# Optimization experiments

Measured on AMD Instinct MI355X. Metric: run time of the kernel, lower is better.

The kernel has to match this reference:

```python
import jax, jax.numpy as jnp
import numpy as np

B, T, J, D = 64, 2048, 128, 512


def setup_inputs() -> dict:
    key = jax.random.key(0)
    k1, k2, k3, k4 = jax.random.split(key, 4)
    question = jax.random.normal(k1, (B, J, D), dtype=jnp.float32)
    context = jax.random.normal(k2, (B, T, D), dtype=jnp.float32)
    question_len = jax.random.randint(k3, (B,), 1, J + 1, dtype=jnp.int32)
    context_len = jax.random.randint(k4, (B,), 1, T + 1, dtype=jnp.int32)
    weight = jnp.ones((D, 1), dtype=jnp.float32)  # initializer='ones'
    return {"question": question, "context": context,
            "question_len": question_len, "context_len": context_len,
            "weight": weight}


def reference(question, context, question_len, context_len, weight):
    # Original computes sum_d context[b,t,d]*question[b,j,d]*w[d] via a
    # broadcast [B,T,J,D] intermediate; reformulated as a batched GEMM.
    w = weight[:, 0]                                   # [D]
    sim = jnp.einsum('btd,bjd->btj', context * w, question)  # [B,T,J]
    Jm = question.shape[1]
    Tm = context.shape[1]
    q_mask = (jnp.arange(Jm) < question_len[:, None]).astype(jnp.float32)  # [B,J]
    c_mask = (jnp.arange(Tm) < context_len[:, None]).astype(jnp.float32)   # [B,T]
    mask = c_mask[:, :, None] * q_mask[:, None, :]     # [B,T,J]
    neg = jnp.finfo(jnp.float32).min
    sim = sim + neg * (1.0 - mask)
    attn = jax.nn.softmax(sim, axis=1)                 # softmax over context axis T
    return jnp.sum(attn * mask, axis=2)[..., None]     # [B,T,1]
```

## Files before the change

### kernel.cpp

```cpp
#include <hip/hip_runtime.h>
#include <stdint.h>
#include <math.h>

#define BB 64
#define TT 2048
#define JJ 128
#define DD 512
#define BK 32

typedef short short8 __attribute__((ext_vector_type(8)));
typedef float f32x4 __attribute__((ext_vector_type(4)));

typedef const __attribute__((address_space(1))) uint32_t glb_u32;
typedef __attribute__((address_space(3))) uint32_t lds_u32;

__device__ __forceinline__ void dma16(const void* g, void* l) {
  __builtin_amdgcn_global_load_lds((glb_u32*)g, (lds_u32*)l, 16, 0, 0);
}

__device__ inline unsigned pk_hi(float a, float b) {
  return __builtin_amdgcn_perm(__float_as_uint(b), __float_as_uint(a), 0x07060302u);
}
__device__ inline float truncbf(float x) {
  return __uint_as_float(__float_as_uint(x) & 0xFFFF0000u);
}
__device__ inline void pack8(float4 a, float4 b, uint4& h, uint4& l) {
  h = make_uint4(pk_hi(a.x, a.y), pk_hi(a.z, a.w), pk_hi(b.x, b.y), pk_hi(b.z, b.w));
  float l0 = a.x - truncbf(a.x), l1 = a.y - truncbf(a.y);
  float l2 = a.z - truncbf(a.z), l3 = a.w - truncbf(a.w);
  float l4 = b.x - truncbf(b.x), l5 = b.y - truncbf(b.y);
  float l6 = b.z - truncbf(b.z), l7 = b.w - truncbf(b.w);
  l = make_uint4(pk_hi(l0, l1), pk_hi(l2, l3), pk_hi(l4, l5), pk_hi(l6, l7));
}
__device__ inline short8 bc8(uint4 u) { return __builtin_bit_cast(short8, u); }

__global__ __launch_bounds__(256)
void qpack_kernel(const float* __restrict__ Qm, const float* __restrict__ w,
                  uint4* __restrict__ Qhi, uint4* __restrict__ Qlo) {
  const int gid = blockIdx.x * 256 + threadIdx.x;
  const int c = gid & 3;
  const int ks = (gid >> 2) & 15;
  const int j = (gid >> 6) & 127;
  const int b = gid >> 13;
  const float* qp = Qm + (((size_t)b * JJ + j) * DD) + ks * BK + c * 8;
  const float* wp = w + ks * BK + c * 8;
  float4 a = *(const float4*)qp;
  float4 bq = *(const float4*)(qp + 4);
  float4 wa = *(const float4*)wp;
  float4 wb = *(const float4*)(wp + 4);
  a.x *= wa.x; a.y *= wa.y; a.z *= wa.z; a.w *= wa.w;
  bq.x *= wb.x; bq.y *= wb.y; bq.z *= wb.z; bq.w *= wb.w;
  uint4 h, l;
  pack8(a, bq, h, l);
  const int slot = j * 4 + (c ^ ((j >> 1) & 3));
  const size_t o = ((size_t)(b * 16 + ks)) * 512 + slot;
  Qhi[o] = h;
  Qlo[o] = l;
}

__global__ __launch_bounds__(256, 3)
void sim_gemm_mfma(const uint4* __restrict__ Qhi, const uint4* __restrict__ Qlo,
                   const float* __restrict__ Cm, const int* __restrict__ qlen,
                   const int* __restrict__ clen, float* __restrict__ S) {
  __shared__ uint4 Ah[512];
  __shared__ uint4 Al[512];
  __shared__ uint4 Cl[1024];

  const int id = blockIdx.x;
  const int nid = (id & 7) * 128 + (id >> 3);
  const int b = nid >> 4;
  const int t0 = (nid & 15) * 128;

  const int cl = clen[b];
  if (t0 >= cl) return;
  const int ql = qlen[b];

  const int tid = threadIdx.x;
  const int lane = tid & 63;
  const int wv = tid >> 6;

  const uint4* qh_src = Qhi + (size_t)b * 8192 + wv * 128 + lane;
  const uint4* ql_src = Qlo + (size_t)b * 8192 + wv * 128 + lane;
  char* ah_dst = (char*)Ah + wv * 2048;
  char* al_dst = (char*)Al + wv * 2048;
  const int crow = wv * 32 + (lane >> 3);
  const int cch = (lane & 7) ^ ((lane >> 3) & 7);
  const float* c_src = Cm + ((size_t)b * TT + t0 + crow) * DD + cch * 4;
  char* cl_dst = (char*)Cl + wv * 4096;

  const int wm = (wv & 1) * 64;
  const int wn = (wv >> 1) * 64;
  const int l15 = lane & 15;
  const int q = lane >> 4;
  const int fchunk = q ^ ((l15 >> 1) & 3);
  const int swl = l15 & 7;

  bool mact[4];
#pragma unroll
  for (int i = 0; i < 4; i++) mact[i] = (wm + i * 16) < ql;
  const bool any_m = mact[0];

  int aslot[4];
#pragma unroll
  for (int i = 0; i < 4; i++) aslot[i] = (wm + i * 16 + l15) * 4 + fchunk;

  f32x4 acc[4][4] = {};

  for (int ks = 0; ks < 16; ks++) {
    __syncthreads();
#pragma unroll
    for (int s = 0; s < 2; s++) {
      dma16(qh_src + ks * 512 + s * 64, ah_dst + s * 1024);
      dma16(ql_src + ks * 512 + s * 64, al_dst + s * 1024);
    }
#pragma unroll
    for (int s = 0; s < 4; s++) {
      dma16(c_src + (size_t)ks * BK + s * 8 * DD, cl_dst + s * 1024);
    }
    __syncthreads();

    if (!any_m) continue;

    short8 bh[4], bl[4];
#pragma unroll
    for (int ni = 0; ni < 4; ni++) {
      const int row = wn + ni * 16 + l15;
      float4 v0 = __builtin_bit_cast(float4, Cl[row * 8 + ((2 * q) ^ swl)]);
      float4 v1 = __builtin_bit_cast(float4, Cl[row * 8 + ((2 * q + 1) ^ swl)]);
      uint4 h, l;
      pack8(v0, v1, h, l);
      bh[ni] = bc8(h);
      bl[ni] = bc8(l);
    }
#pragma unroll
    for (int mi = 0; mi < 4; mi++) {
      if (!mact[mi]) continue;
      short8 ah = bc8(Ah[aslot[mi]]);
      short8 al = bc8(Al[aslot[mi]]);
#pragma unroll
      for (int ni = 0; ni < 4; ni++) {
        acc[mi][ni] = __builtin_amdgcn_mfma_f32_16x16x32_bf16(ah, bh[ni], acc[mi][ni], 0, 0, 0);
        acc[mi][ni] = __builtin_amdgcn_mfma_f32_16x16x32_bf16(al, bh[ni], acc[mi][ni], 0, 0, 0);
        acc[mi][ni] = __builtin_amdgcn_mfma_f32_16x16x32_bf16(ah, bl[ni], acc[mi][ni], 0, 0, 0);
      }
    }
  }

#pragma unroll
  for (int mi = 0; mi < 4; mi++) {
    if (!mact[mi]) continue;
#pragma unroll
    for (int ni = 0; ni < 4; ni++) {
      const int j = wm + mi * 16 + q * 4;
      const int t = t0 + wn + ni * 16 + l15;
      float* dst = S + ((size_t)b * JJ + j) * TT + t;
      dst[0 * TT] = acc[mi][ni][0];
      dst[1 * TT] = acc[mi][ni][1];
      dst[2 * TT] = acc[mi][ni][2];
      dst[3 * TT] = acc[mi][ni][3];
    }
  }
}

__global__ __launch_bounds__(256)
void softmax_stats_kernel(const float* __restrict__ S, const int* __restrict__ qlen,
                          const int* __restrict__ clen, float* __restrict__ m_out,
                          float* __restrict__ r_out) {
  const int j = blockIdx.x;
  const int b = blockIdx.y;
  if (j >= qlen[b]) return;
  const int cl = clen[b];
  const int tid = threadIdx.x;
  const float4* row = (const float4*)(S + ((size_t)b * JJ + j) * TT);

  const float NEG = -3.4e38f;
  float4 v0 = make_float4(NEG, NEG, NEG, NEG);
  float4 v1 = make_float4(NEG, NEG, NEG, NEG);
  const int t0 = tid * 4;
  const int t1 = (tid + 256) * 4;
  if (t0 < cl) v0 = row[tid];
  if (t1 < cl) v1 = row[tid + 256];

  float m = NEG;
  m = fmaxf(m, (t0 + 0 < cl) ? v0.x : NEG);
  m = fmaxf(m, (t0 + 1 < cl) ? v0.y : NEG);
  m = fmaxf(m, (t0 + 2 < cl) ? v0.z : NEG);
  m = fmaxf(m, (t0 + 3 < cl) ? v0.w : NEG);
  m = fmaxf(m, (t1 + 0 < cl) ? v1.x : NEG);
  m = fmaxf(m, (t1 + 1 < cl) ? v1.y : NEG);
  m = fmaxf(m, (t1 + 2 < cl) ? v1.z : NEG);
  m = fmaxf(m, (t1 + 3 < cl) ? v1.w : NEG);

  __shared__ float red[8];
#pragma unroll
  for (int off = 32; off > 0; off >>= 1) m = fmaxf(m, __shfl_down(m, off));
  if ((tid & 63) == 0) red[tid >> 6] = m;
  __syncthreads();
  m = fmaxf(fmaxf(red[0], red[1]), fmaxf(red[2], red[3]));

  float s = 0.f;
  s += (t0 + 0 < cl) ? __expf(v0.x - m) : 0.f;
  s += (t0 + 1 < cl) ? __expf(v0.y - m) : 0.f;
  s += (t0 + 2 < cl) ? __expf(v0.z - m) : 0.f;
  s += (t0 + 3 < cl) ? __expf(v0.w - m) : 0.f;
  s += (t1 + 0 < cl) ? __expf(v1.x - m) : 0.f;
  s += (t1 + 1 < cl) ? __expf(v1.y - m) : 0.f;
  s += (t1 + 2 < cl) ? __expf(v1.z - m) : 0.f;
  s += (t1 + 3 < cl) ? __expf(v1.w - m) : 0.f;
#pragma unroll
  for (int off = 32; off > 0; off >>= 1) s += __shfl_down(s, off);
  if ((tid & 63) == 0) red[4 + (tid >> 6)] = s;
  __syncthreads();
  s = red[4] + red[5] + red[6] + red[7];

  if (tid == 0) {
    m_out[(size_t)b * JJ + j] = m;
    r_out[(size_t)b * JJ + j] = 1.f / s;
  }
}

__global__ __launch_bounds__(256)
void out_kernel(const float* __restrict__ S, const float* __restrict__ m_arr,
                const float* __restrict__ r_arr, const int* __restrict__ qlen,
                const int* __restrict__ clen, float* __restrict__ out) {
  const int b = blockIdx.y;
  const int t = blockIdx.x * 256 + threadIdx.x;
  const int ql = qlen[b];
  const int cl = clen[b];

  __shared__ float lm[JJ];
  __shared__ float lr[JJ];
  if (threadIdx.x < ql) {
    lm[threadIdx.x] = m_arr[(size_t)b * JJ + threadIdx.x];
    lr[threadIdx.x] = r_arr[(size_t)b * JJ + threadIdx.x];
  }
  __syncthreads();

  float acc = 0.f;
  if (t < cl) {
    const float* col = S + (size_t)b * JJ * TT + t;
#pragma unroll 4
    for (int j = 0; j < ql; j++) {
      acc += __expf(col[(size_t)j * TT] - lm[j]) * lr[j];
    }
  }
  out[(size_t)b * TT + t] = acc;
}

extern "C" void kernel_launch(void* const* d_in, const int* in_sizes, int n_in,
                              void* d_out, int out_size, void* d_ws, size_t ws_size,
                              hipStream_t stream) {
  const float* question = (const float*)d_in[0];
  const float* context  = (const float*)d_in[1];
  const int*   qlen     = (const int*)d_in[2];
  const int*   clen     = (const int*)d_in[3];
  const float* weight   = (const float*)d_in[4];
  float* out = (float*)d_out;

  float* S = (float*)d_ws;
  float* m_arr = S + (size_t)BB * JJ * TT;
  float* r_arr = m_arr + (size_t)BB * JJ;
  uint4* Qhi = (uint4*)(r_arr + (size_t)BB * JJ);
  uint4* Qlo = Qhi + (size_t)BB * 16 * 512;

  qpack_kernel<<<dim3(2048), 256, 0, stream>>>(question, weight, Qhi, Qlo);
  sim_gemm_mfma<<<dim3(1024), 256, 0, stream>>>(Qhi, Qlo, context, qlen, clen, S);
  softmax_stats_kernel<<<dim3(JJ, BB), 256, 0, stream>>>(S, qlen, clen, m_arr, r_arr);
  out_kernel<<<dim3(TT / 256, BB), 256, 0, stream>>>(S, m_arr, r_arr, qlen, clen, out);
}
```

Measured before the change: 393.6 us.

## Load GEMM operands directly from global into registers, dropping LDS staging

The similarity GEMM no longer stages Q and context tiles through shared memory with async global-to-LDS copies and barriers. Each wave now loads its own MFMA fragments straight from global memory into registers. The Q pre-pack kernel writes fragments in the exact per-lane order the MFMA expects, so those reads are contiguous. This removes the block-wide synchronisation and lets waves with no valid question rows exit early. In exchange, context data that two waves share is read twice from global or cache, context loads are less coalesced, and launch bounds drop to 1, which may raise register use and change occupancy.

```diff
diff --git a/kernel.cpp b/kernel.cpp
--- a/kernel.cpp
+++ b/kernel.cpp
@@ -10,13 +10,6 @@
 
 typedef short short8 __attribute__((ext_vector_type(8)));
 typedef float f32x4 __attribute__((ext_vector_type(4)));
-
-typedef const __attribute__((address_space(1))) uint32_t glb_u32;
-typedef __attribute__((address_space(3))) uint32_t lds_u32;
-
-__device__ __forceinline__ void dma16(const void* g, void* l) {
-  __builtin_amdgcn_global_load_lds((glb_u32*)g, (lds_u32*)l, 16, 0, 0);
-}
 
 __device__ inline unsigned pk_hi(float a, float b) {
   return __builtin_amdgcn_perm(__float_as_uint(b), __float_as_uint(a), 0x07060302u);
@@ -38,11 +31,15 @@
 void qpack_kernel(const float* __restrict__ Qm, const float* __restrict__ w,
                   uint4* __restrict__ Qhi, uint4* __restrict__ Qlo) {
   const int gid = blockIdx.x * 256 + threadIdx.x;
-  const int c = gid & 3;
-  const int ks = (gid >> 2) & 15;
-  const int j = (gid >> 6) & 127;
+  const int lane = gid & 63;
+  const int mi = (gid >> 6) & 3;
+  const int str = (gid >> 8) & 1;
+  const int ks = (gid >> 9) & 15;
   const int b = gid >> 13;
-  const float* qp = Qm + (((size_t)b * JJ + j) * DD) + ks * BK + c * 8;
+  const int j = str * 64 + mi * 16 + (lane & 15);
+  const int c = lane >> 4;
+
+  const float* qp = Qm + ((size_t)b * JJ + j) * DD + ks * BK + c * 8;
   const float* wp = w + ks * BK + c * 8;
   float4 a = *(const float4*)qp;
   float4 bq = *(const float4*)(qp + 4);
@@ -52,20 +49,14 @@
   bq.x *= wb.x; bq.y *= wb.y; bq.z *= wb.z; bq.w *= wb.w;
   uint4 h, l;
   pack8(a, bq, h, l);
-  const int slot = j * 4 + (c ^ ((j >> 1) & 3));
-  const size_t o = ((size_t)(b * 16 + ks)) * 512 + slot;
-  Qhi[o] = h;
-  Qlo[o] = l;
-}
-
-__global__ __launch_bounds__(256, 3)
+  Qhi[gid] = h;
+  Qlo[gid] = l;
+}
+
+__global__ __launch_bounds__(256, 1)
 void sim_gemm_mfma(const uint4* __restrict__ Qhi, const uint4* __restrict__ Qlo,
                    const float* __restrict__ Cm, const int* __restrict__ qlen,
                    const int* __restrict__ clen, float* __restrict__ S) {
-  __shared__ uint4 Ah[512];
-  __shared__ uint4 Al[512];
-  __shared__ uint4 Cl[1024];
-
   const int id = blockIdx.x;
   const int nid = (id & 7) * 128 + (id >> 3);
   const int b = nid >> 4;
@@ -78,65 +69,51 @@
   const int tid = threadIdx.x;
   const int lane = tid & 63;
   const int wv = tid >> 6;
-
-  const uint4* qh_src = Qhi + (size_t)b * 8192 + wv * 128 + lane;
-  const uint4* ql_src = Qlo + (size_t)b * 8192 + wv * 128 + lane;
-  char* ah_dst = (char*)Ah + wv * 2048;
-  char* al_dst = (char*)Al + wv * 2048;
-  const int crow = wv * 32 + (lane >> 3);
-  const int cch = (lane & 7) ^ ((lane >> 3) & 7);
-  const float* c_src = Cm + ((size_t)b * TT + t0 + crow) * DD + cch * 4;
-  char* cl_dst = (char*)Cl + wv * 4096;
-
   const int wm = (wv & 1) * 64;
   const int wn = (wv >> 1) * 64;
   const int l15 = lane & 15;
   const int q = lane >> 4;
-  const int fchunk = q ^ ((l15 >> 1) & 3);
-  const int swl = l15 & 7;
 
   bool mact[4];
 #pragma unroll
   for (int i = 0; i < 4; i++) mact[i] = (wm + i * 16) < ql;
-  const bool any_m = mact[0];
-
-  int aslot[4];
-#pragma unroll
-  for (int i = 0; i < 4; i++) aslot[i] = (wm + i * 16 + l15) * 4 + fchunk;
+  if (!mact[0]) return;
+
+  const uint4* ahp = Qhi + (size_t)b * 8192 + (wv & 1) * 256 + lane;
+  const uint4* alp = Qlo + (size_t)b * 8192 + (wv & 1) * 256 + lane;
+  const float* cb = Cm + ((size_t)b * TT + t0 + wn + l15) * DD + q * 8;
 
   f32x4 acc[4][4] = {};
 
   for (int ks = 0; ks < 16; ks++) {
-    __syncthreads();
-#pragma unroll
-    for (int s = 0; s < 2; s++) {
-      dma16(qh_src + ks * 512 + s * 64, ah_dst + s * 1024);
-      dma16(ql_src + ks * 512 + s * 64, al_dst + s * 1024);
-    }
-#pragma unroll
-    for (int s = 0; s < 4; s++) {
-      dma16(c_src + (size_t)ks * BK + s * 8 * DD, cl_dst + s * 1024);
-    }
-    __syncthreads();
-
-    if (!any_m) continue;
-
+    float4 cv0[4], cv1[4];
+#pragma unroll
+    for (int ni = 0; ni < 4; ni++) {
+      const float* cp = cb + ni * 16 * DD + ks * BK;
+      cv0[ni] = *(const float4*)cp;
+      cv1[ni] = *(const float4*)(cp + 4);
+    }
+    uint4 ahv[4], alv[4];
+#pragma unroll
+    for (int mi = 0; mi < 4; mi++) {
+      if (mact[mi]) {
+        ahv[mi] = ahp[ks * 512 + mi * 64];
+        alv[mi] = alp[ks * 512 + mi * 64];
+      }
+    }
     short8 bh[4], bl[4];
 #pragma unroll
     for (int ni = 0; ni < 4; ni++) {
-      const int row = wn + ni * 16 + l15;
-      float4 v0 = __builtin_bit_cast(float4, Cl[row * 8 + ((2 * q) ^ swl)]);
-      float4 v1 = __builtin_bit_cast(float4, Cl[row * 8 + ((2 * q + 1) ^ swl)]);
       uint4 h, l;
-      pack8(v0, v1, h, l);
+      pack8(cv0[ni], cv1[ni], h, l);
       bh[ni] = bc8(h);
       bl[ni] = bc8(l);
     }
 #pragma unroll
     for (int mi = 0; mi < 4; mi++) {
       if (!mact[mi]) continue;
-      short8 ah = bc8(Ah[aslot[mi]]);
-      short8 al = bc8(Al[aslot[mi]]);
+      short8 ah = bc8(ahv[mi]);
+      short8 al = bc8(alv[mi]);
 #pragma unroll
       for (int ni = 0; ni < 4; ni++) {
         acc[mi][ni] = __builtin_amdgcn_mfma_f32_16x16x32_bf16(ah, bh[ni], acc[mi][ni], 0, 0, 0);
```

New measurement: 397.6 us. About the same (+1.0%).

## Fuse per-tile softmax max/sum into GEMM epilogue and merge partials online

Applied to the files above, without the earlier changes.

The GEMM epilogue now computes per-tile row max and exp-sum from the accumulators using shuffles and shared memory, writing (max,sum) partials per 128-column tile. A small merge kernel combines the partials with an online-softmax rescale, replacing the stats kernel that re-read the full similarity matrix. This removes one full pass over S from global memory, at the cost of extra epilogue work, barriers, and register pressure in the GEMM kernel.

```diff
diff --git a/kernel.cpp b/kernel.cpp
--- a/kernel.cpp
+++ b/kernel.cpp
@@ -33,6 +33,17 @@
   l = make_uint4(pk_hi(l0, l1), pk_hi(l2, l3), pk_hi(l4, l5), pk_hi(l6, l7));
 }
 __device__ inline short8 bc8(uint4 u) { return __builtin_bit_cast(short8, u); }
+
+__device__ __forceinline__ float redmax16(float v) {
+#pragma unroll
+  for (int off = 1; off < 16; off <<= 1) v = fmaxf(v, __shfl_xor(v, off));
+  return v;
+}
+__device__ __forceinline__ float redsum16(float v) {
+#pragma unroll
+  for (int off = 1; off < 16; off <<= 1) v += __shfl_xor(v, off);
+  return v;
+}
 
 __global__ __launch_bounds__(256)
 void qpack_kernel(const float* __restrict__ Qm, const float* __restrict__ w,
@@ -61,15 +72,17 @@
 __global__ __launch_bounds__(256, 3)
 void sim_gemm_mfma(const uint4* __restrict__ Qhi, const uint4* __restrict__ Qlo,
                    const float* __restrict__ Cm, const int* __restrict__ qlen,
-                   const int* __restrict__ clen, float* __restrict__ S) {
-  __shared__ uint4 Ah[512];
-  __shared__ uint4 Al[512];
+                   const int* __restrict__ clen, float* __restrict__ S,
+                   float2* __restrict__ Part) {
+  __shared__ uint4 Ahi[512];
+  __shared__ uint4 Alo[512];
   __shared__ uint4 Cl[1024];
 
   const int id = blockIdx.x;
   const int nid = (id & 7) * 128 + (id >> 3);
   const int b = nid >> 4;
-  const int t0 = (nid & 15) * 128;
+  const int tile = nid & 15;
+  const int t0 = tile * 128;
 
   const int cl = clen[b];
   if (t0 >= cl) return;
@@ -81,8 +94,8 @@
 
   const uint4* qh_src = Qhi + (size_t)b * 8192 + wv * 128 + lane;
   const uint4* ql_src = Qlo + (size_t)b * 8192 + wv * 128 + lane;
-  char* ah_dst = (char*)Ah + wv * 2048;
-  char* al_dst = (char*)Al + wv * 2048;
+  char* ah_dst = (char*)Ahi + wv * 2048;
+  char* al_dst = (char*)Alo + wv * 2048;
   const int crow = wv * 32 + (lane >> 3);
   const int cch = (lane & 7) ^ ((lane >> 3) & 7);
   const float* c_src = Cm + ((size_t)b * TT + t0 + crow) * DD + cch * 4;
@@ -135,8 +148,8 @@
 #pragma unroll
     for (int mi = 0; mi < 4; mi++) {
       if (!mact[mi]) continue;
-      short8 ah = bc8(Ah[aslot[mi]]);
-      short8 al = bc8(Al[aslot[mi]]);
+      short8 ah = bc8(Ahi[aslot[mi]]);
+      short8 al = bc8(Alo[aslot[mi]]);
 #pragma unroll
       for (int ni = 0; ni < 4; ni++) {
         acc[mi][ni] = __builtin_amdgcn_mfma_f32_16x16x32_bf16(ah, bh[ni], acc[mi][ni], 0, 0, 0);
@@ -160,63 +173,87 @@
       dst[3 * TT] = acc[mi][ni][3];
     }
   }
+
+  bool cv[4];
+#pragma unroll
+  for (int ni = 0; ni < 4; ni++) cv[ni] = (t0 + wn + ni * 16 + l15) < cl;
+
+  const float NEG = -3.4e38f;
+  __syncthreads();
+  float* Pm = (float*)Ahi;
+  float* Ps = Pm + 256;
+  const int half = wv >> 1;
+
+  float mrow[4][4];
+#pragma unroll
+  for (int mi = 0; mi < 4; mi++) {
+#pragma unroll
+    for (int r = 0; r < 4; r++) {
+      float m = NEG;
+#pragma unroll
+      for (int ni = 0; ni < 4; ni++) m = fmaxf(m, cv[ni] ? acc[mi][ni][r] : NEG);
+      mrow[mi][r] = redmax16(m);
+    }
+  }
+  if (l15 == 0) {
+#pragma unroll
+    for (int mi = 0; mi < 4; mi++)
+#pragma unroll
+      for (int r = 0; r < 4; r++)
+        Pm[(wm + mi * 16 + q * 4 + r) * 2 + half] = mrow[mi][r];
+  }
+  __syncthreads();
+  float srow[4][4];
+#pragma unroll
+  for (int mi = 0; mi < 4; mi++) {
+#pragma unroll
+    for (int r = 0; r < 4; r++) {
+      const int row = wm + mi * 16 + q * 4 + r;
+      const float mf = fmaxf(Pm[row * 2 + 0], Pm[row * 2 + 1]);
+      float s = 0.f;
+#pragma unroll
+      for (int ni = 0; ni < 4; ni++)
+        s += cv[ni] ? __expf(acc[mi][ni][r] - mf) : 0.f;
+      srow[mi][r] = redsum16(s);
+    }
+  }
+  if (l15 == 0) {
+#pragma unroll
+    for (int mi = 0; mi < 4; mi++)
+#pragma unroll
+      for (int r = 0; r < 4; r++)
+        Ps[(wm + mi * 16 + q * 4 + r) * 2 + half] = srow[mi][r];
+  }
+  __syncthreads();
+  if (tid < JJ) {
+    const float m = fmaxf(Pm[tid * 2 + 0], Pm[tid * 2 + 1]);
+    const float s = Ps[tid * 2 + 0] + Ps[tid * 2 + 1];
+    Part[((size_t)b * 16 + tile) * JJ + tid] = make_float2(m, s);
+  }
 }
 
 __global__ __launch_bounds__(256)
-void softmax_stats_kernel(const float* __restrict__ S, const int* __restrict__ qlen,
-                          const int* __restrict__ clen, float* __restrict__ m_out,
-                          float* __restrict__ r_out) {
-  const int j = blockIdx.x;
-  const int b = blockIdx.y;
+void merge_kernel(const float2* __restrict__ Part, const int* __restrict__ qlen,
+                  const int* __restrict__ clen, float* __restrict__ m_out,
+                  float* __restrict__ r_out) {
+  const int gid = blockIdx.x * 256 + threadIdx.x;
+  const int b = gid >> 7;
+  const int j = gid & 127;
   if (j >= qlen[b]) return;
-  const int cl = clen[b];
-  const int tid = threadIdx.x;
-  const float4* row = (const float4*)(S + ((size_t)b * JJ + j) * TT);
-
-  const float NEG = -3.4e38f;
-  float4 v0 = make_float4(NEG, NEG, NEG, NEG);
-  float4 v1 = make_float4(NEG, NEG, NEG, NEG);
-  const int t0 = tid * 4;
-  const int t1 = (tid + 256) * 4;
-  if (t0 < cl) v0 = row[tid];
-  if (t1 < cl) v1 = row[tid + 256];
-
-  float m = NEG;
-  m = fmaxf(m, (t0 + 0 < cl) ? v0.x : NEG);
-  m = fmaxf(m, (t0 + 1 < cl) ? v0.y : NEG);
-  m = fmaxf(m, (t0 + 2 < cl) ? v0.z : NEG);
-  m = fmaxf(m, (t0 + 3 < cl) ? v0.w : NEG);
-  m = fmaxf(m, (t1 + 0 < cl) ? v1.x : NEG);
-  m = fmaxf(m, (t1 + 1 < cl) ? v1.y : NEG);
-  m = fmaxf(m, (t1 + 2 < cl) ? v1.z : NEG);
-  m = fmaxf(m, (t1 + 3 < cl) ? v1.w : NEG);
-
-  __shared__ float red[8];
-#pragma unroll
-  for (int off = 32; off > 0; off >>= 1) m = fmaxf(m, __shfl_down(m, off));
-  if ((tid & 63) == 0) red[tid >> 6] = m;
-  __syncthreads();
-  m = fmaxf(fmaxf(red[0], red[1]), fmaxf(red[2], red[3]));
-
+  const int nt = (clen[b] + 127) >> 7;
+  float m = -3.4e38f;
   float s = 0.f;
-  s += (t0 + 0 < cl) ? __expf(v0.x - m) : 0.f;
-  s += (t0 + 1 < cl) ? __expf(v0.y - m) : 0.f;
-  s += (t0 + 2 < cl) ? __expf(v0.z - m) : 0.f;
-  s += (t0 + 3 < cl) ? __expf(v0.w - m) : 0.f;
-  s += (t1 + 0 < cl) ? __expf(v1.x - m) : 0.f;
-  s += (t1 + 1 < cl) ? __expf(v1.y - m) : 0.f;
-  s += (t1 + 2 < cl) ? __expf(v1.z - m) : 0.f;
-  s += (t1 + 3 < cl) ? __expf(v1.w - m) : 0.f;
-#pragma unroll
-  for (int off = 32; off > 0; off >>= 1) s += __shfl_down(s, off);
-  if ((tid & 63) == 0) red[4 + (tid >> 6)] = s;
-  __syncthreads();
-  s = red[4] + red[5] + red[6] + red[7];
-
-  if (tid == 0) {
-    m_out[(size_t)b * JJ + j] = m;
-    r_out[(size_t)b * JJ + j] = 1.f / s;
-  }
+  for (int i = 0; i < nt; i++) {
+    const float2 p = Part[((size_t)b * 16 + i) * JJ + j];
+    if (p.x > m) {
+      s = s * __expf(m - p.x) + p.y;
+      m = p.x;
+    } else {
+      s += p.y * __expf(p.x - m);
+    }
+  }
+  m_out[(size_t)b * JJ + j] = m;
+  r_out[(size_t)b * JJ + j] = 1.f / s;
 }
 
 __global__ __launch_bounds__(256)
@@ -262,9 +299,10 @@
   float* r_arr = m_arr + (size_t)BB * JJ;
   uint4* Qhi = (uint4*)(r_arr + (size_t)BB * JJ);
   uint4* Qlo = Qhi + (size_t)BB * 16 * 512;
+  float2* Part = (float2*)(Qlo + (size_t)BB * 16 * 512);
 
   qpack_kernel<<<dim3(2048), 256, 0, stream>>>(question, weight, Qhi, Qlo);
-  sim_gemm_mfma<<<dim3(1024), 256, 0, stream>>>(Qhi, Qlo, context, qlen, clen, S);
-  softmax_stats_kernel<<<dim3(JJ, BB), 256, 0, stream>>>(S, qlen, clen, m_arr, r_arr);
+  sim_gemm_mfma<<<dim3(1024), 256, 0, stream>>>(Qhi, Qlo, context, qlen, clen, S, Part);
+  merge_kernel<<<dim3(32), 256, 0, stream>>>(Part, qlen, clen, m_arr, r_arr);
   out_kernel<<<dim3(TT / 256, BB), 256, 0, stream>>>(S, m_arr, r_arr, qlen, clen, out);
 }
```

New measurement: 398.6 us. About the same (+1.3%).
